# Performance work log

Hardware: AMD Instinct MI355X
Metric: run time of the kernel (lower is better)

The kernel has to match this reference:

```python
import jax, jax.numpy as jnp
import numpy as np

BIG_CONST = 1000000.0
LN_EPS = 1e-5

B, S, D = 2, 1024, 1024
N, H = 16, D // 16            # n_head, d_head
POS_LEN = 2 * S - 1


def setup_inputs() -> dict:
    key = jax.random.key(0)
    ks = jax.random.split(key, 16)
    std_qkv = np.sqrt(1.0 / float(D + N * H))   # EinsumLayer init: 1/sqrt(fan_in+fan_out)
    std_post = np.sqrt(1.0 / float(N * H + D))
    return {
        "q": jax.random.normal(ks[0], (B, S, D), jnp.float32),
        "k": jax.random.normal(ks[1], (B, S, D), jnp.float32),
        "v": jax.random.normal(ks[2], (B, S, D), jnp.float32),
        "pos_enc": jax.random.normal(ks[3], (POS_LEN, D), jnp.float32),
        "attn_mask": jax.random.randint(ks[4], (B, 1, 1, S), 0, 2, jnp.int32),
        "q_w": jax.random.normal(ks[5], (D, N, H), jnp.float32) * std_qkv,
        "k_w": jax.random.normal(ks[6], (D, N, H), jnp.float32) * std_qkv,
        "k_b": jnp.zeros((N, H), jnp.float32),
        "v_w": jax.random.normal(ks[7], (D, N, H), jnp.float32) * std_qkv,
        "v_b": jnp.zeros((N, H), jnp.float32),
        "r_w_bias": jax.random.uniform(ks[8], (N, 1, H), jnp.float32, 0.0, 0.1),
        "r_r_bias": jax.random.uniform(ks[9], (N, 1, H), jnp.float32, 0.0, 0.1),
        "r_kernel": jax.random.uniform(ks[10], (N, D, H), jnp.float32, 0.0, 0.1),
        "post_w": jax.random.normal(ks[11], (N, H, D), jnp.float32) * std_post,
        "post_b": jnp.zeros((D,), jnp.float32),
        "ln_g": jnp.ones((D,), jnp.float32),
        "ln_b": jnp.zeros((D,), jnp.float32),
    }


def reference(q, k, v, pos_enc, attn_mask, q_w, k_w, k_b, v_w, v_b,
              r_w_bias, r_r_bias, r_kernel, post_w, post_b, ln_g, ln_b):
    input_q = q
    d_head = q_w.shape[-1]
    normalizer = 1.0 / np.sqrt(d_head)

    # head projections -> [B, N, L, H]
    qh = jnp.einsum('bld,dnh->bnlh', q, q_w)
    kh = jnp.einsum('bld,dnh->bnlh', k, k_w) + k_b[None, :, None, :] * 0 + jnp.transpose(k_b, (0, 1))[None, :, None, :] * 0 + k_b.reshape(1, k_b.shape[0], 1, k_b.shape[1])
    kh = jnp.einsum('bld,dnh->bnlh', k, k_w) + k_b.reshape(1, -1, 1, d_head)
    vh = jnp.einsum('bld,dnh->bnlh', v, v_w) + v_b.reshape(1, -1, 1, d_head)

    # content score: (q + r_w_bias) @ k^T * normalizer   [B,N,S,S]
    content = jnp.einsum('bnqh,bnkh->bnqk', qh + r_w_bias[None], kh) * normalizer

    # positional term (rel_shift with shift=0): r = pos_enc @ r_kernel -> [N, P, H]
    r = jnp.einsum('pd,ndh->nph', pos_enc, r_kernel)
    pos_scores = jnp.einsum('bnqh,nph->bnqp', qh + r_r_bias[None], r) * normalizer
    # shift=0 => reshape-swap + narrow + reshape-back is an exact identity; then narrow to k_len
    k_len = kh.shape[-2]
    pos_term = pos_scores[..., :k_len]

    attn_score = (content + pos_term).astype(jnp.float32)
    attn_score = attn_score - BIG_CONST * attn_mask.astype(jnp.float32)
    attn_dist = jax.nn.softmax(attn_score, axis=-1)

    out = jnp.einsum('bnqk,bnkh->bnqh', attn_dist, vh)          # [B,N,S,H]
    attn_out = jnp.einsum('bnlh,nhd->bld', out, post_w) + post_b

    x = input_q + attn_out
    mu = jnp.mean(x, axis=-1, keepdims=True)
    var = jnp.mean(jnp.square(x - mu), axis=-1, keepdims=True)
    return (x - mu) / jnp.sqrt(var + LN_EPS) * ln_g + ln_b
```

## Files before the change

### kernel.cpp

```cpp
#include <hip/hip_runtime.h>
#include <cstddef>
#include <cstdint>

typedef unsigned short u16;
typedef unsigned int   u32;

#define S_LEN  1024
#define NHEAD  16
#define HDIM   64
#define DMODEL 1024
#define NORMSC 0.125f
#define BIGC   1000000.0f
#define LOG2E  1.44269504088896f
#define SC2    (0.125f * 1.44269504088896f)

typedef __bf16 bf16x8 __attribute__((ext_vector_type(8)));
typedef float  f32x4  __attribute__((ext_vector_type(4)));

#define MFMA16(a, b, c) __builtin_amdgcn_mfma_f32_16x16x32_bf16((a), (b), (c), 0, 0, 0)

__device__ __forceinline__ u16 f2bf(float f) {
    u32 u = __float_as_uint(f);
    u32 r = (u + 0x7fffu + ((u >> 16) & 1u)) >> 16;
    return (u16)r;
}
__device__ __forceinline__ float bf2f(u32 v) {
    return __uint_as_float(v << 16);
}
__device__ __forceinline__ float4 unp4(uint2 u) {
    float4 f;
    f.x = bf2f(u.x & 0xffffu); f.y = bf2f(u.x >> 16);
    f.z = bf2f(u.y & 0xffffu); f.w = bf2f(u.y >> 16);
    return f;
}
__device__ __forceinline__ void async16(const void* g, void* l) {
    __builtin_amdgcn_global_load_lds(
        (__attribute__((address_space(1))) void*)(g),
        (__attribute__((address_space(3))) void*)(l), 16, 0, 0);
}

__global__ __launch_bounds__(256) void prep_all(
    const float* q, const float* k, const float* v, const float* pos,
    const float* qw, const float* kw, const float* vw, const float* pw, const float* rk,
    u16* qbf, u16* kbf, u16* vbf, u16* posb,
    u16* qwT, u16* kwT, u16* vwT, u16* pwT, u16* WrT)
{
    __shared__ float tb[32][33];
    const int bid = blockIdx.x, tid = threadIdx.x;
    if (bid < 7168) {
        const float* s; u16* d; int base;
        if (bid < 2048)      { s = q;   d = qbf;  base = bid; }
        else if (bid < 4096) { s = k;   d = kbf;  base = bid - 2048; }
        else if (bid < 6144) { s = v;   d = vbf;  base = bid - 4096; }
        else                 { s = pos; d = posb; base = bid - 6144; }
        const int i = base * 1024 + tid * 4;
        const float4 val = *(const float4*)&s[i];
        uint2 o;
        o.x = (u32)f2bf(val.x) | ((u32)f2bf(val.y) << 16);
        o.y = (u32)f2bf(val.z) | ((u32)f2bf(val.w) << 16);
        *(uint2*)&d[i] = o;
        return;
    }
    const int t = bid - 7168;
    const float* in; u16* out; int ild, r0, c0;
    if (t < 4096) {
        const int ts = t & 1023;
        if (t < 1024)      { in = qw; out = qwT; }
        else if (t < 2048) { in = kw; out = kwT; }
        else if (t < 3072) { in = vw; out = vwT; }
        else               { in = pw; out = pwT; }
        ild = 1024;
        r0 = (ts >> 5) * 32; c0 = (ts & 31) * 32;
    } else {
        const int ts = t - 4096;
        const int n = ts >> 6, tt = ts & 63;
        in = rk + (size_t)n * 65536; out = WrT + (size_t)n * 65536;
        ild = 64;
        r0 = (tt >> 1) * 32; c0 = (tt & 1) * 32;
    }
    const int tx = tid & 31, ty = tid >> 5;
    for (int i = ty; i < 32; i += 8)
        tb[i][tx] = in[(size_t)(r0 + i) * ild + c0 + tx];
    __syncthreads();
    for (int i = ty; i < 32; i += 8)
        out[(size_t)(c0 + i) * 1024 + r0 + tx] = f2bf(tb[tx][i]);
}

struct GJ { const u16* A; const u16* Bt; u16* C; int M; int k0; int klen; };

__global__ __launch_bounds__(256) void gemm_p(
    GJ j0, GJ j1, GJ j2, GJ j3, GJ j4, GJ j5, GJ j6, GJ j7)
{
    GJ g;
    switch (blockIdx.z) {
        case 0: g = j0; break; case 1: g = j1; break;
        case 2: g = j2; break; case 3: g = j3; break;
        case 4: g = j4; break; case 5: g = j5; break;
        case 6: g = j6; break; default: g = j7;
    }
    const int bm = blockIdx.y * 128;
    if (bm >= g.M) return;
    const int bn = blockIdx.x * 128;
    __shared__ u16 As[4096];
    __shared__ u16 Bs[4096];
    const int tid = threadIdx.x;
    const int w = tid >> 6, lane = tid & 63;
    const int wm = (w >> 1) * 64, wn = (w & 1) * 64;
    const int l15 = lane & 15, l16 = lane >> 4;
    f32x4 acc[4][4] = {};
    const char* Ab = (const char*)g.A;
    const char* Bb = (const char*)g.Bt;
    const int kend = g.k0 + g.klen;
    for (int k0 = g.k0; k0 < kend; k0 += 32) {
        __syncthreads();
#pragma unroll
        for (int i = 0; i < 2; ++i) {
            const int m = (i * 4 + w) * 1024 + lane * 16;
            const int r = m >> 6, cb = m & 63;
            async16(Ab + ((size_t)(bm + r) * 1024 + k0) * 2 + cb, (char*)As + m);
            async16(Bb + ((size_t)(bn + r) * 1024 + k0) * 2 + cb, (char*)Bs + m);
        }
        __syncthreads();
        bf16x8 af[4], bfr[4];
#pragma unroll
        for (int i = 0; i < 4; ++i)
            af[i] = *(const bf16x8*)&As[(wm + i * 16 + l15) * 32 + l16 * 8];
#pragma unroll
        for (int j = 0; j < 4; ++j)
            bfr[j] = *(const bf16x8*)&Bs[(wn + j * 16 + l15) * 32 + l16 * 8];
#pragma unroll
        for (int i = 0; i < 4; ++i)
#pragma unroll
            for (int j = 0; j < 4; ++j)
                acc[i][j] = MFMA16(af[i], bfr[j], acc[i][j]);
    }
#pragma unroll
    for (int i = 0; i < 4; ++i)
#pragma unroll
        for (int j = 0; j < 4; ++j) {
            const int c = bn + wn + j * 16 + l15;
#pragma unroll
            for (int rg = 0; rg < 4; ++rg) {
                const int m = bm + wm + i * 16 + l16 * 4 + rg;
                g.C[(size_t)m * 1024 + c] = f2bf(acc[i][j][rg]);
            }
        }
}

__global__ __launch_bounds__(256) void prep2(
    const u16* pk0, const u16* pk1, const u16* pr0, const u16* pr1,
    const u16* pv0, const u16* pv1, const u16* pq0, const u16* pq1,
    const float* kbi, const float* vbi, const float* rwb, const float* rrb,
    const int* mask, u16* keff, float* cc, u16* vT, u16* qhb)
{
    __shared__ float tb[32][33];
    const int bid = blockIdx.x, tid = threadIdx.x;
    if (bid < 2048) {
        const int t = bid * 256 + tid;
        const int row = t >> 4, li = t & 15;
        const int n = (row >> 10) & 15, kk = row & 1023, b = row >> 14;
        const size_t mi = ((size_t)(b * 1024 + kk)) * 1024 + n * 64 + li * 4;
        const size_t pi = ((size_t)kk) * 1024 + n * 64 + li * 4;
        const float4 k0v = unp4(*(const uint2*)&pk0[mi]);
        const float4 k1v = unp4(*(const uint2*)&pk1[mi]);
        const float4 r0v = unp4(*(const uint2*)&pr0[pi]);
        const float4 r1v = unp4(*(const uint2*)&pr1[pi]);
        const float4 kb4 = *(const float4*)&kbi[n * 64 + li * 4];
        float4 kv, rv;
        kv.x = k0v.x + k1v.x + kb4.x; kv.y = k0v.y + k1v.y + kb4.y;
        kv.z = k0v.z + k1v.z + kb4.z; kv.w = k0v.w + k1v.w + kb4.w;
        rv.x = r0v.x + r1v.x; rv.y = r0v.y + r1v.y;
        rv.z = r0v.z + r1v.z; rv.w = r0v.w + r1v.w;
        const float4 w1 = *(const float4*)&rwb[n * 64 + li * 4];
        const float4 w2 = *(const float4*)&rrb[n * 64 + li * 4];
        float s = w1.x * kv.x + w1.y * kv.y + w1.z * kv.z + w1.w * kv.w
                + w2.x * rv.x + w2.y * rv.y + w2.z * rv.z + w2.w * rv.w;
        uint2 o;
        o.x = (u32)f2bf(kv.x + rv.x) | ((u32)f2bf(kv.y + rv.y) << 16);
        o.y = (u32)f2bf(kv.z + rv.z) | ((u32)f2bf(kv.w + rv.w) << 16);
        *(uint2*)&keff[(size_t)row * 64 + li * 4] = o;
#pragma unroll
        for (int m = 1; m < 16; m <<= 1) s += __shfl_xor(s, m);
        if (li == 0)
            cc[row] = LOG2E * (NORMSC * s - BIGC * (float)mask[b * 1024 + kk]);
        return;
    }
    if (bid < 4096) {
        const int t = bid - 2048;
        const int head = t >> 6, tt = t & 63;
        const int b = head >> 4, n = head & 15;
        const int r0 = (tt >> 1) * 32, c0 = (tt & 1) * 32;
        const int tx = tid & 31, ty = tid >> 5;
        const float vb = vbi[n * 64 + c0 + tx];
        for (int i = ty; i < 32; i += 8) {
            const size_t idx = ((size_t)(b * 1024 + r0 + i)) * 1024 + n * 64 + c0 + tx;
            tb[i][tx] = bf2f(pv0[idx]) + bf2f(pv1[idx]) + vb;
        }
        __syncthreads();
        u16* out = vT + (size_t)head * 65536;
        for (int i = ty; i < 32; i += 8)
            out[(size_t)(c0 + i) * 1024 + r0 + tx] = f2bf(tb[tx][i]);
        return;
    }
    const int t = bid - 4096;
    const int e = t * 1024 + tid * 4;
    const int m = e >> 10, c = e & 1023;
    const float4 a = unp4(*(const uint2*)&pq0[e]);
    const float4 b4 = unp4(*(const uint2*)&pq1[e]);
    uint2 o;
    o.x = (u32)f2bf(a.x + b4.x) | ((u32)f2bf(a.y + b4.y) << 16);
    o.y = (u32)f2bf(a.z + b4.z) | ((u32)f2bf(a.w + b4.w) << 16);
    const int b2 = m >> 10, l = m & 1023, n = c >> 6, h = c & 63;
    *(uint2*)&qhb[(((size_t)(b2 * NHEAD + n)) * 1024 + l) * 64 + h] = o;
}

__global__ __launch_bounds__(128) void attn_mfma(
    const u16* qb, const u16* kb, const u16* vtb, const float* ccomb, u16* O)
{
    __shared__ u16   Ks[4096];
    __shared__ u16   Vs[4096];
    __shared__ __bf16 Ps[2][1024];
    const int tid = threadIdx.x;
    const int w = tid >> 6, lane = tid & 63;
    const int l15 = lane & 15, l16 = lane >> 4;
    const int head = blockIdx.x >> 5;
    const int q0 = (blockIdx.x & 31) * 32;
    const int b = head >> 4, n = head & 15;
    const size_t hoff = (size_t)head * 65536;
    const u16* qh = qb + hoff;
    const char* khc = (const char*)(kb + hoff);
    const char* vtc = (const char*)(vtb + hoff);
    const float* cc = ccomb + head * 1024;
    __bf16* Pw = Ps[w];

    bf16x8 qf[2];
    {
        const size_t rb = ((size_t)(q0 + w * 16 + l15)) * 64 + l16 * 8;
        qf[0] = *(const bf16x8*)&qh[rb];
        qf[1] = *(const bf16x8*)&qh[rb + 32];
    }
    f32x4 Oacc[4] = {};
    float lsum[4] = {};

    for (int kc = 0; kc < 16; ++kc) {
        __syncthreads();
#pragma unroll
        for (int i = 0; i < 4; ++i) {
            const int r = w * 32 + i * 8 + (lane >> 3);
            const int c = lane & 7;
            async16(khc + kc * 8192 + r * 128 + (((c + r) & 7) << 4),
                    (char*)Ks + r * 128 + c * 16);
            async16(vtc + (size_t)r * 2048 + kc * 128 + (((c + r) & 7) << 4),
                    (char*)Vs + r * 128 + c * 16);
        }
        __syncthreads();

        f32x4 sc[4];
#pragma unroll
        for (int j = 0; j < 4; ++j) {
            const int rk2 = j * 16 + l15;
            const int base = rk2 * 64;
            f32x4 a = {0.f, 0.f, 0.f, 0.f};
            a = MFMA16(qf[0], *(const bf16x8*)&Ks[base + (((l16 - rk2) & 7) << 3)], a);
            a = MFMA16(qf[1], *(const bf16x8*)&Ks[base + (((l16 + 4 - rk2) & 7) << 3)], a);
            const float cadd = cc[kc * 64 + j * 16 + l15];
            sc[j] = a * SC2 + cadd;
        }
#pragma unroll
        for (int j = 0; j < 4; ++j) {
            const int cg = j * 2 + (l15 >> 3);
#pragma unroll
            for (int rg = 0; rg < 4; ++rg) {
                const float p = exp2f(sc[j][rg]);
                lsum[rg] += p;
                const int row = l16 * 4 + rg;
                Pw[row * 64 + (((cg - row) & 7) << 3) + (l15 & 7)] = (__bf16)p;
            }
        }
        bf16x8 pf[2];
#pragma unroll
        for (int f = 0; f < 2; ++f)
            pf[f] = *(const bf16x8*)&Pw[l15 * 64 + (((f * 4 + l16 - l15) & 7) << 3)];
#pragma unroll
        for (int t4 = 0; t4 < 4; ++t4) {
#pragma unroll
            for (int f = 0; f < 2; ++f) {
                const int vr = t4 * 16 + l15;
                const int ch = f * 4 + l16;
                const bf16x8 vf = *(const bf16x8*)&Vs[vr * 64 + (((ch - vr) & 7) << 3)];
                Oacc[t4] = MFMA16(pf[f], vf, Oacc[t4]);
            }
        }
    }
    float inv[4];
#pragma unroll
    for (int rg = 0; rg < 4; ++rg) {
        float s = lsum[rg];
#pragma unroll
        for (int m = 1; m < 16; m <<= 1) s += __shfl_xor(s, m);
        inv[rg] = 1.0f / s;
    }
#pragma unroll
    for (int t4 = 0; t4 < 4; ++t4) {
#pragma unroll
        for (int rg = 0; rg < 4; ++rg) {
            const int srow = q0 + w * 16 + l16 * 4 + rg;
            const int col = n * 64 + t4 * 16 + l15;
            O[((size_t)b * 1024 + srow) * 1024 + col] = f2bf(Oacc[t4][rg] * inv[rg]);
        }
    }
}

__global__ __launch_bounds__(256) void ln_kernel(
    const u16* __restrict__ p0, const u16* __restrict__ p1,
    const u16* __restrict__ p2, const u16* __restrict__ p3,
    const float* __restrict__ resid, const float* __restrict__ pb,
    const float* __restrict__ g, const float* __restrict__ bb,
    float* __restrict__ out)
{
    const int row = blockIdx.x;
    const int tid = threadIdx.x;
    const size_t i = (size_t)row * DMODEL + tid * 4;
    const float4 a0 = unp4(*(const uint2*)&p0[i]);
    const float4 a1 = unp4(*(const uint2*)&p1[i]);
    const float4 a2 = unp4(*(const uint2*)&p2[i]);
    const float4 a3 = unp4(*(const uint2*)&p3[i]);
    const float4 rr = *(const float4*)&resid[i];
    const float4 pv = *(const float4*)&pb[tid * 4];
    float4 v;
    v.x = a0.x + a1.x + a2.x + a3.x + rr.x + pv.x;
    v.y = a0.y + a1.y + a2.y + a3.y + rr.y + pv.y;
    v.z = a0.z + a1.z + a2.z + a3.z + rr.z + pv.z;
    v.w = a0.w + a1.w + a2.w + a3.w + rr.w + pv.w;
    float s1 = v.x + v.y + v.z + v.w;
    float s2 = v.x * v.x + v.y * v.y + v.z * v.z + v.w * v.w;
#pragma unroll
    for (int off = 32; off; off >>= 1) {
        s1 += __shfl_down(s1, off);
        s2 += __shfl_down(s2, off);
    }
    __shared__ float rb[8];
    if ((tid & 63) == 0) { rb[tid >> 6] = s1; rb[4 + (tid >> 6)] = s2; }
    __syncthreads();
    if (tid == 0) {
        rb[0] = rb[0] + rb[1] + rb[2] + rb[3];
        rb[4] = rb[4] + rb[5] + rb[6] + rb[7];
    }
    __syncthreads();
    s1 = rb[0]; s2 = rb[4];
    const float mu = s1 * (1.0f / DMODEL);
    const float var = s2 * (1.0f / DMODEL) - mu * mu;
    const float rstd = rsqrtf(var + 1e-5f);
    const float4 gv = *(const float4*)&g[tid * 4];
    const float4 bv = *(const float4*)&bb[tid * 4];
    float4 o;
    o.x = (v.x - mu) * rstd * gv.x + bv.x;
    o.y = (v.y - mu) * rstd * gv.y + bv.y;
    o.z = (v.z - mu) * rstd * gv.z + bv.z;
    o.w = (v.w - mu) * rstd * gv.w + bv.w;
    *(float4*)&out[i] = o;
}

extern "C" void kernel_launch(void* const* d_in, const int* in_sizes, int n_in,
                              void* d_out, int out_size, void* d_ws, size_t ws_size,
                              hipStream_t stream)
{
    (void)in_sizes; (void)n_in; (void)out_size; (void)ws_size;
    const float* q   = (const float*)d_in[0];
    const float* k   = (const float*)d_in[1];
    const float* v   = (const float*)d_in[2];
    const float* pos = (const float*)d_in[3];
    const int*   msk = (const int*)d_in[4];
    const float* qw  = (const float*)d_in[5];
    const float* kw  = (const float*)d_in[6];
    const float* kbi = (const float*)d_in[7];
    const float* vw  = (const float*)d_in[8];
    const float* vbi = (const float*)d_in[9];
    const float* rwb = (const float*)d_in[10];
    const float* rrb = (const float*)d_in[11];
    const float* rk  = (const float*)d_in[12];
    const float* pw  = (const float*)d_in[13];
    const float* pb  = (const float*)d_in[14];
    const float* lg  = (const float*)d_in[15];
    const float* lb  = (const float*)d_in[16];
    float* out = (float*)d_out;

    float* fb = (float*)d_ws;
    float* cc   = fb;
    u16* us   = (u16*)(cc + 32768);
    u16* qbf  = us;
    u16* kbf  = qbf + 2097152;
    u16* vbf  = kbf + 2097152;
    u16* posb = vbf + 2097152;
    u16* qwT  = posb + 1048576;
    u16* kwT  = qwT + 1048576;
    u16* vwT  = kwT + 1048576;
    u16* pwT  = vwT + 1048576;
    u16* WrT  = pwT + 1048576;
    u16* qhb  = WrT + 1048576;
    u16* keffb= qhb + 2097152;
    u16* vTb  = keffb + 2097152;
    u16* pq0  = vTb + 2097152;
    u16* pq1  = pq0 + 2097152;
    u16* pk0  = pq1 + 2097152;
    u16* pk1  = pk0 + 2097152;
    u16* pv0  = pk1 + 2097152;
    u16* pv1  = pv0 + 2097152;
    u16* pr0  = pv1 + 2097152;
    u16* pr1  = pr0 + 1048576;
    u16* po0  = pr1 + 1048576;
    u16* po1  = po0 + 2097152;
    u16* po2  = po1 + 2097152;
    u16* po3  = po2 + 2097152;
    u16* Obf  = qbf;

    dim3 blk(256);
    prep_all<<<12288, blk, 0, stream>>>(q, k, v, pos, qw, kw, vw, pw, rk,
                                        qbf, kbf, vbf, posb, qwT, kwT, vwT, pwT, WrT);

    GJ jq0 = {qbf,  qwT, pq0, 2048, 0,   512};
    GJ jq1 = {qbf,  qwT, pq1, 2048, 512, 512};
    GJ jk0 = {kbf,  kwT, pk0, 2048, 0,   512};
    GJ jk1 = {kbf,  kwT, pk1, 2048, 512, 512};
    GJ jv0 = {vbf,  vwT, pv0, 2048, 0,   512};
    GJ jv1 = {vbf,  vwT, pv1, 2048, 512, 512};
    GJ jp0 = {posb, WrT, pr0, 1024, 0,   512};
    GJ jp1 = {posb, WrT, pr1, 1024, 512, 512};
    gemm_p<<<dim3(8, 16, 8), blk, 0, stream>>>(jq0, jq1, jk0, jk1, jv0, jv1, jp0, jp1);

    prep2<<<6144, blk, 0, stream>>>(pk0, pk1, pr0, pr1, pv0, pv1, pq0, pq1,
                                    kbi, vbi, rwb, rrb, msk, keffb, cc, vTb, qhb);

    attn_mfma<<<1024, dim3(128), 0, stream>>>(qhb, keffb, vTb, cc, Obf);

    GJ jo0 = {Obf, pwT, po0, 2048, 0,   256};
    GJ jo1 = {Obf, pwT, po1, 2048, 256, 256};
    GJ jo2 = {Obf, pwT, po2, 2048, 512, 256};
    GJ jo3 = {Obf, pwT, po3, 2048, 768, 256};
    gemm_p<<<dim3(8, 16, 4), blk, 0, stream>>>(jo0, jo1, jo2, jo3, jo0, jo0, jo0, jo0);

    ln_kernel<<<2048, blk, 0, stream>>>(po0, po1, po2, po3, q, pb, lg, lb, out);
}
```

Before: 224.5 us.

## Double-buffer LDS tiles in GEMM and attention kernels to overlap loads

New measurement: 212.8 us. 1.05x faster.

```diff
diff --git a/kernel.cpp b/kernel.cpp
--- a/kernel.cpp
+++ b/kernel.cpp
@@ -101,8 +101,8 @@
     const int bm = blockIdx.y * 128;
     if (bm >= g.M) return;
     const int bn = blockIdx.x * 128;
-    __shared__ u16 As[4096];
-    __shared__ u16 Bs[4096];
+    __shared__ u16 As[2][4096];
+    __shared__ u16 Bs[2][4096];
     const int tid = threadIdx.x;
     const int w = tid >> 6, lane = tid & 63;
     const int wm = (w >> 1) * 64, wn = (w & 1) * 64;
@@ -111,28 +111,37 @@
     const char* Ab = (const char*)g.A;
     const char* Bb = (const char*)g.Bt;
     const int kend = g.k0 + g.klen;
+    const int m0 = w * 1024 + lane * 16;
+    const int m1 = (4 + w) * 1024 + lane * 16;
+    const int r0w = m0 >> 6, cb0 = m0 & 63;
+    const int r1w = m1 >> 6, cb1 = m1 & 63;
+    async16(Ab + ((size_t)(bm + r0w) * 1024 + g.k0) * 2 + cb0, (char*)As[0] + m0);
+    async16(Bb + ((size_t)(bn + r0w) * 1024 + g.k0) * 2 + cb0, (char*)Bs[0] + m0);
+    async16(Ab + ((size_t)(bm + r1w) * 1024 + g.k0) * 2 + cb1, (char*)As[0] + m1);
+    async16(Bb + ((size_t)(bn + r1w) * 1024 + g.k0) * 2 + cb1, (char*)Bs[0] + m1);
+    int buf = 0;
     for (int k0 = g.k0; k0 < kend; k0 += 32) {
         __syncthreads();
-#pragma unroll
-        for (int i = 0; i < 2; ++i) {
-            const int m = (i * 4 + w) * 1024 + lane * 16;
-            const int r = m >> 6, cb = m & 63;
-            async16(Ab + ((size_t)(bm + r) * 1024 + k0) * 2 + cb, (char*)As + m);
-            async16(Bb + ((size_t)(bn + r) * 1024 + k0) * 2 + cb, (char*)Bs + m);
-        }
-        __syncthreads();
+        const int kn = k0 + 32;
+        if (kn < kend) {
+            async16(Ab + ((size_t)(bm + r0w) * 1024 + kn) * 2 + cb0, (char*)As[buf ^ 1] + m0);
+            async16(Bb + ((size_t)(bn + r0w) * 1024 + kn) * 2 + cb0, (char*)Bs[buf ^ 1] + m0);
+            async16(Ab + ((size_t)(bm + r1w) * 1024 + kn) * 2 + cb1, (char*)As[buf ^ 1] + m1);
+            async16(Bb + ((size_t)(bn + r1w) * 1024 + kn) * 2 + cb1, (char*)Bs[buf ^ 1] + m1);
+        }
         bf16x8 af[4], bfr[4];
 #pragma unroll
         for (int i = 0; i < 4; ++i)
-            af[i] = *(const bf16x8*)&As[(wm + i * 16 + l15) * 32 + l16 * 8];
+            af[i] = *(const bf16x8*)&As[buf][(wm + i * 16 + l15) * 32 + l16 * 8];
 #pragma unroll
         for (int j = 0; j < 4; ++j)
-            bfr[j] = *(const bf16x8*)&Bs[(wn + j * 16 + l15) * 32 + l16 * 8];
+            bfr[j] = *(const bf16x8*)&Bs[buf][(wn + j * 16 + l15) * 32 + l16 * 8];
 #pragma unroll
         for (int i = 0; i < 4; ++i)
 #pragma unroll
             for (int j = 0; j < 4; ++j)
                 acc[i][j] = MFMA16(af[i], bfr[j], acc[i][j]);
+        buf ^= 1;
     }
 #pragma unroll
     for (int i = 0; i < 4; ++i)
@@ -217,8 +226,8 @@
 __global__ __launch_bounds__(128) void attn_mfma(
     const u16* qb, const u16* kb, const u16* vtb, const float* ccomb, u16* O)
 {
-    __shared__ u16   Ks[4096];
-    __shared__ u16   Vs[4096];
+    __shared__ u16   Ks[2][4096];
+    __shared__ u16   Vs[2][4096];
     __shared__ __bf16 Ps[2][1024];
     const int tid = threadIdx.x;
     const int w = tid >> 6, lane = tid & 63;
@@ -242,27 +251,38 @@
     f32x4 Oacc[4] = {};
     float lsum[4] = {};
 
+    const int sr0 = w * 32 + (lane >> 3);
+    const int sc0 = lane & 7;
+#pragma unroll
+    for (int i = 0; i < 4; ++i) {
+        const int r = sr0 + i * 8;
+        async16(khc + r * 128 + (((sc0 + r) & 7) << 4), (char*)Ks[0] + r * 128 + sc0 * 16);
+        async16(vtc + (size_t)r * 2048 + (((sc0 + r) & 7) << 4), (char*)Vs[0] + r * 128 + sc0 * 16);
+    }
+    int buf = 0;
     for (int kc = 0; kc < 16; ++kc) {
         __syncthreads();
-#pragma unroll
-        for (int i = 0; i < 4; ++i) {
-            const int r = w * 32 + i * 8 + (lane >> 3);
-            const int c = lane & 7;
-            async16(khc + kc * 8192 + r * 128 + (((c + r) & 7) << 4),
-                    (char*)Ks + r * 128 + c * 16);
-            async16(vtc + (size_t)r * 2048 + kc * 128 + (((c + r) & 7) << 4),
-                    (char*)Vs + r * 128 + c * 16);
-        }
-        __syncthreads();
-
+        if (kc < 15) {
+            const int kn = kc + 1;
+#pragma unroll
+            for (int i = 0; i < 4; ++i) {
+                const int r = sr0 + i * 8;
+                async16(khc + kn * 8192 + r * 128 + (((sc0 + r) & 7) << 4),
+                        (char*)Ks[buf ^ 1] + r * 128 + sc0 * 16);
+                async16(vtc + (size_t)r * 2048 + kn * 128 + (((sc0 + r) & 7) << 4),
+                        (char*)Vs[buf ^ 1] + r * 128 + sc0 * 16);
+            }
+        }
+        const u16* Kb = Ks[buf];
+        const u16* Vb = Vs[buf];
         f32x4 sc[4];
 #pragma unroll
         for (int j = 0; j < 4; ++j) {
             const int rk2 = j * 16 + l15;
             const int base = rk2 * 64;
             f32x4 a = {0.f, 0.f, 0.f, 0.f};
-            a = MFMA16(qf[0], *(const bf16x8*)&Ks[base + (((l16 - rk2) & 7) << 3)], a);
-            a = MFMA16(qf[1], *(const bf16x8*)&Ks[base + (((l16 + 4 - rk2) & 7) << 3)], a);
+            a = MFMA16(qf[0], *(const bf16x8*)&Kb[base + (((l16 - rk2) & 7) << 3)], a);
+            a = MFMA16(qf[1], *(const bf16x8*)&Kb[base + (((l16 + 4 - rk2) & 7) << 3)], a);
             const float cadd = cc[kc * 64 + j * 16 + l15];
             sc[j] = a * SC2 + cadd;
         }
@@ -287,10 +307,11 @@
             for (int f = 0; f < 2; ++f) {
                 const int vr = t4 * 16 + l15;
                 const int ch = f * 4 + l16;
-                const bf16x8 vf = *(const bf16x8*)&Vs[vr * 64 + (((ch - vr) & 7) << 3)];
+                const bf16x8 vf = *(const bf16x8*)&Vb[vr * 64 + (((ch - vr) & 7) << 3)];
                 Oacc[t4] = MFMA16(pf[f], vf, Oacc[t4]);
             }
         }
+        buf ^= 1;
     }
     float inv[4];
 #pragma unroll
```
